# Kernel optimization log

Hardware: AMD Instinct MI355X
Metric: run time of the kernel (lower is better)

## Reference

```python
import jax, jax.numpy as jnp
import numpy as np
from jax import lax

NMS_RADIUS = 4  # module default


def conv2d(x, w, b, pad):
    # x: [B,C,H,W], w: [O,I,kh,kw]
    y = lax.conv_general_dilated(x, w, window_strides=(1, 1),
                                 padding=[(pad, pad), (pad, pad)],
                                 dimension_numbers=('NCHW', 'OIHW', 'NCHW'))
    return y + b[None, :, None, None]


def max_pool(x, r):
    # x: [B,H,W]; kernel (2r+1)x(2r+1), stride 1, pad r (torch pads with -inf)
    k = 2 * r + 1
    return lax.reduce_window(x, -jnp.inf, lax.max,
                             window_dimensions=(1, k, k),
                             window_strides=(1, 1, 1),
                             padding=[(0, 0), (r, r), (r, r)])


def simple_nms(scores, r):
    zeros = jnp.zeros_like(scores)
    max_mask = scores == max_pool(scores, r)
    for _ in range(2):
        supp_mask = max_pool(max_mask.astype(scores.dtype), r) > 0
        supp_scores = jnp.where(supp_mask, zeros, scores)
        new_max_mask = supp_scores == max_pool(supp_scores, r)
        max_mask = max_mask | (new_max_mask & ~supp_mask)
    return jnp.where(max_mask, scores, zeros)


def setup_inputs() -> dict:
    key = jax.random.key(0)
    ks = jax.random.split(key, 7)
    B, Hc, Wc = 16, 60, 80
    x = jax.random.normal(ks[0], (B, 512, Hc, Wc), dtype=jnp.float32)
    wPa = jax.random.normal(ks[1], (256, 512, 3, 3), dtype=jnp.float32) * 0.02
    bPa = jax.random.normal(ks[2], (256,), dtype=jnp.float32) * 0.02
    wPd = jax.random.normal(ks[3], (128, 256, 3, 3), dtype=jnp.float32) * 0.02
    bPd = jax.random.normal(ks[4], (128,), dtype=jnp.float32) * 0.02
    wPg = jax.random.normal(ks[5], (65, 128, 1, 1), dtype=jnp.float32) * 0.02
    bPg = jax.random.normal(ks[6], (65,), dtype=jnp.float32) * 0.02
    return {'x': x, 'wPa': wPa, 'bPa': bPa, 'wPd': wPd, 'bPd': bPd,
            'wPg': wPg, 'bPg': bPg}


def reference(x, wPa, bPa, wPd, bPd, wPg, bPg):
    h1 = jax.nn.relu(conv2d(x, wPa, bPa, pad=1))          # [B,256,Hc,Wc]
    h2 = jax.nn.relu(conv2d(h1, wPd, bPd, pad=1))         # [B,128,Hc,Wc]
    logits = conv2d(h2, wPg, bPg, pad=0)                  # [B,65,Hc,Wc]
    scores = jax.nn.softmax(logits, axis=1)[:, :-1]       # [B,64,Hc,Wc]
    b, _, h, w = scores.shape
    # pixel-unshuffle 8x8 cells -> full resolution
    scores = scores.transpose(0, 2, 3, 1).reshape(b, h, w, 8, 8)
    scores = scores.transpose(0, 1, 3, 2, 4).reshape(b, h * 8, w * 8)
    return simple_nms(scores, NMS_RADIUS)
```

## Files before the change

### kernel.cpp

```cpp
#include <hip/hip_runtime.h>
#include <hip/hip_bf16.h>
#include <math.h>


#define B_      16
#define HC      60
#define WC      80
#define PIX     (HC * WC)
#define HF      480
#define WF      640
#define IMG     (HF * WF)
#define NPIX    (B_ * IMG)

typedef double f64x4 __attribute__((ext_vector_type(4)));

__device__ __forceinline__ int clampi(int v, int lo, int hi) {
    return v < lo ? lo : (v > hi ? hi : v);
}

__global__ __launch_bounds__(256) void cvt_f32_f64(const float* __restrict__ s,
                                                   double* __restrict__ d, int n)
{
    int i = blockIdx.x * 256 + threadIdx.x;
    if (i < n) d[i] = (double)s[i];
}

__global__ __launch_bounds__(256) void prep_w(const float* __restrict__ w,
                                              double* __restrict__ wT,
                                              int CIN, int n)
{
    int i = blockIdx.x * 256 + threadIdx.x;
    if (i >= n) return;
    int cin9 = CIN * 9;
    int oc   = i / cin9;
    int rem  = i - oc * cin9;
    int ic   = rem / 9;
    int dydx = rem - ic * 9;
    size_t dst = ((size_t)((oc >> 4) * (CIN >> 2) + (ic >> 2)) * 9 + dydx) * 64
               + (ic & 3) * 16 + (oc & 15);
    wT[dst] = (double)w[i];
}

template <int CIN, typename TIN, bool RELU>
__global__ __launch_bounds__(256, 4) void conv3x3_mfma(
    const TIN* __restrict__ in,
    const double* __restrict__ wT,
    const double* __restrict__ bias,
    double* __restrict__ out)
{
    const int COUT  = (CIN == 512) ? 256 : 128;
    const int NCH   = CIN / 4;
    const int ytile = blockIdx.x;
    const int ocb   = blockIdx.y;
    const int oc0   = ocb * 16;
    const int b     = blockIdx.z;
    const int tid   = threadIdx.x;
    const int wv    = tid >> 6;
    const int lane  = tid & 63;
    const int q     = lane >> 4;
    const int c     = lane & 15;
    const int y0    = ytile * 4;

    in  += (size_t)b * CIN  * PIX;
    out += (size_t)b * COUT * PIX;

    int rowL[4], colL[4];
    {
        f64x4 pr = (f64x4){0.0, 0.0, 0.0, 0.0};
        double a1 = (lane < 16) ? (double)(16 * lane) : 0.0;
        double b1 = (lane < 16) ? 1.0 : 0.0;
        pr = __builtin_amdgcn_mfma_f64_16x16x4f64(a1, b1, pr, 0, 0, 0);
        double a2 = (lane < 16) ? 1.0 : 0.0;
        double b2 = (lane < 16) ? (double)lane : 0.0;
        pr = __builtin_amdgcn_mfma_f64_16x16x4f64(a2, b2, pr, 0, 0, 0);
#pragma unroll
        for (int i = 0; i < 4; ++i) {
            int code = (int)pr[i];
            rowL[i] = (code >> 4) & 15;
            colL[i] = code & 15;
        }
    }

    __shared__ double smem[2][2544];

    const double* wchunk = wT + (size_t)ocb * NCH * 576;

    f64x4 acc[5];
#pragma unroll
    for (int t = 0; t < 5; ++t) acc[t] = (f64x4){0.0, 0.0, 0.0, 0.0};

    const int bbase = q * 492 + wv * 82 + c;

    int aOff[8];
#pragma unroll
    for (int j = 0; j < 8; ++j) {
        int i   = tid + j * 256;
        int ick = i / 492;
        int rem = i - ick * 492;
        int ry  = rem / 82;
        int rx  = rem - ry * 82;
        int gy  = y0 - 1 + ry, gx = rx - 1;
        bool ok = (i < 1968) && ((unsigned)gy < (unsigned)HC) && ((unsigned)gx < (unsigned)WC);
        aOff[j] = ok ? (ick * PIX + gy * WC + gx) : -1;
    }

    double ra[8];
    double rw0, rw1, rw2;

#define LOADC(ch)                                                              \
    {                                                                          \
        const int gbase = (ch) * 4 * PIX;                                      \
        _Pragma("unroll")                                                      \
        for (int j = 0; j < 8; ++j)                                            \
            ra[j] = (aOff[j] >= 0) ? (double)in[gbase + aOff[j]] : 0.0;        \
        const double* wp = wchunk + (size_t)(ch) * 576;                        \
        rw0 = wp[tid];                                                         \
        rw1 = wp[256 + tid];                                                   \
        rw2 = (tid < 64) ? wp[512 + tid] : 0.0;                                \
    }

#define STOREC(sel)                                                            \
    {                                                                          \
        double* dst = smem[sel];                                               \
        _Pragma("unroll")                                                      \
        for (int j = 0; j < 7; ++j) dst[tid + j * 256] = ra[j];                \
        if (tid < 176) dst[tid + 1792] = ra[7];                                \
        dst[1968 + tid] = rw0;                                                 \
        dst[1968 + 256 + tid] = rw1;                                           \
        if (tid < 64) dst[1968 + 512 + tid] = rw2;                             \
    }

    LOADC(0);
    STOREC(0);
    LOADC(1);
    __syncthreads();

    for (int chk = 0; chk < NCH; ++chk) {
        const int cur = chk & 1;
        if (chk + 1 < NCH) STOREC(cur ^ 1);
        if (chk + 2 < NCH) LOADC(chk + 2);

        const double* act = smem[cur];
        const double* wl  = smem[cur] + 1968;
#pragma unroll
        for (int dy = 0; dy < 3; ++dy) {
#pragma unroll
            for (int dx = 0; dx < 3; ++dx) {
                double a = wl[(dy * 3 + dx) * 64 + lane];
#pragma unroll
                for (int t = 0; t < 5; ++t) {
                    double bv = act[bbase + dy * 82 + t * 16 + dx];
                    acc[t] = __builtin_amdgcn_mfma_f64_16x16x4f64(a, bv, acc[t], 0, 0, 0);
                }
            }
        }
        if (chk + 1 < NCH) __syncthreads();
    }
#undef LOADC
#undef STOREC

    const int y = y0 + wv;
#pragma unroll
    for (int t = 0; t < 5; ++t) {
#pragma unroll
        for (int i = 0; i < 4; ++i) {
            const int oc = oc0 + rowL[i];
            double v = acc[t][i] + bias[oc];
            if (RELU) v = fmax(v, 0.0);
            out[(size_t)oc * PIX + y * WC + t * 16 + colL[i]] = v;
        }
    }
}

__global__ __launch_bounds__(256) void conv1x1_softmax_f64(
    const double* __restrict__ h2,
    const double* __restrict__ wg,
    const double* __restrict__ bg,
    double* __restrict__ S)
{
    int p = blockIdx.x * 256 + threadIdx.x;
    if (p >= PIX) return;
    const int b = blockIdx.y;
    const double* h2p = h2 + (size_t)b * 128 * PIX + p;
    double* Sb = S + (size_t)b * IMG;

    double l[65];
#pragma unroll
    for (int o = 0; o < 65; ++o) l[o] = bg[o];

    for (int icc = 0; icc < 128; icc += 8) {
        double h[8];
#pragma unroll
        for (int k = 0; k < 8; ++k) h[k] = h2p[(size_t)(icc + k) * PIX];
#pragma unroll
        for (int o = 0; o < 65; ++o) {
            const double* wp = wg + o * 128 + icc;
            l[o] += h[0] * wp[0] + h[1] * wp[1] + h[2] * wp[2] + h[3] * wp[3]
                  + h[4] * wp[4] + h[5] * wp[5] + h[6] * wp[6] + h[7] * wp[7];
        }
    }

    double m = l[0];
#pragma unroll
    for (int o = 1; o < 65; ++o) m = fmax(m, l[o]);
    double s = 0.0;
#pragma unroll
    for (int o = 0; o < 65; ++o) { l[o] = exp(l[o] - m); s += l[o]; }
    double inv = 1.0 / s;

    int y = p / WC, x = p % WC;
#pragma unroll
    for (int cy = 0; cy < 8; ++cy)
#pragma unroll
        for (int cx2 = 0; cx2 < 8; ++cx2)
            Sb[(y * 8 + cy) * WF + x * 8 + cx2] = l[cy * 8 + cx2] * inv;
}

__global__ __launch_bounds__(256) void hmax9_f64(const double* __restrict__ in,
                                                 double* __restrict__ out)
{
    int p = blockIdx.x * 256 + threadIdx.x;
    int x = p % WF;
    const double* row = in + (p - x);
    double m = row[x];
#pragma unroll
    for (int d = 1; d <= 4; ++d) {
        m = fmax(m, row[clampi(x - d, 0, WF - 1)]);
        m = fmax(m, row[clampi(x + d, 0, WF - 1)]);
    }
    out[p] = m;
}

__global__ __launch_bounds__(256) void vmax9_eq(const double* __restrict__ T,
                                                const double* __restrict__ S,
                                                unsigned char* __restrict__ M)
{
    int p = blockIdx.x * 256 + threadIdx.x;
    int y = (p % IMG) / WF;
    double m = T[p];
#pragma unroll
    for (int d = 1; d <= 4; ++d) {
        m = fmax(m, T[p + (clampi(y - d, 0, HF - 1) - y) * WF]);
        m = fmax(m, T[p + (clampi(y + d, 0, HF - 1) - y) * WF]);
    }
    M[p] = (S[p] == m) ? (unsigned char)1 : (unsigned char)0;
}

__global__ __launch_bounds__(256) void hor9_u8(const unsigned char* __restrict__ in,
                                               unsigned char* __restrict__ out)
{
    int p = blockIdx.x * 256 + threadIdx.x;
    int x = p % WF;
    const unsigned char* row = in + (p - x);
    unsigned char m = row[x];
#pragma unroll
    for (int d = 1; d <= 4; ++d) {
        m = m | row[clampi(x - d, 0, WF - 1)];
        m = m | row[clampi(x + d, 0, WF - 1)];
    }
    out[p] = m;
}

__global__ __launch_bounds__(256) void vor9_sup(const unsigned char* __restrict__ T8,
                                                unsigned char* __restrict__ SUP)
{
    int p = blockIdx.x * 256 + threadIdx.x;
    int y = (p % IMG) / WF;
    unsigned char m = T8[p];
#pragma unroll
    for (int d = 1; d <= 4; ++d) {
        m = m | T8[p + (clampi(y - d, 0, HF - 1) - y) * WF];
        m = m | T8[p + (clampi(y + d, 0, HF - 1) - y) * WF];
    }
    SUP[p] = m;
}

__global__ __launch_bounds__(256) void hmax9_supp(const double* __restrict__ S,
                                                  const unsigned char* __restrict__ SUP,
                                                  double* __restrict__ T)
{
    int p = blockIdx.x * 256 + threadIdx.x;
    int x = p % WF;
    int base = p - x;
    double m = SUP[p] ? 0.0 : S[p];
#pragma unroll
    for (int d = 1; d <= 4; ++d) {
        int i1 = base + clampi(x - d, 0, WF - 1);
        int i2 = base + clampi(x + d, 0, WF - 1);
        m = fmax(m, SUP[i1] ? 0.0 : S[i1]);
        m = fmax(m, SUP[i2] ? 0.0 : S[i2]);
    }
    T[p] = m;
}

__global__ __launch_bounds__(256) void vmax9_newmask(const double* __restrict__ T,
                                                     const double* __restrict__ S,
                                                     const unsigned char* __restrict__ SUP,
                                                     unsigned char* __restrict__ M)
{
    int p = blockIdx.x * 256 + threadIdx.x;
    int y = (p % IMG) / WF;
    double m = T[p];
#pragma unroll
    for (int d = 1; d <= 4; ++d) {
        m = fmax(m, T[p + (clampi(y - d, 0, HF - 1) - y) * WF]);
        m = fmax(m, T[p + (clampi(y + d, 0, HF - 1) - y) * WF]);
    }
    unsigned char nw = (!SUP[p] && S[p] == m) ? 1 : 0;
    M[p] = M[p] | nw;
}

__global__ __launch_bounds__(256) void final_mask(const double* __restrict__ S,
                                                  const unsigned char* __restrict__ M,
                                                  float* __restrict__ out)
{
    int p = blockIdx.x * 256 + threadIdx.x;
    out[p] = M[p] ? (float)S[p] : 0.f;
}

extern "C" void kernel_launch(void* const* d_in, const int* in_sizes, int n_in,
                              void* d_out, int out_size, void* d_ws, size_t ws_size,
                              hipStream_t stream)
{
    const float* x   = (const float*)d_in[0];
    const float* wPa = (const float*)d_in[1];
    const float* bPa = (const float*)d_in[2];
    const float* wPd = (const float*)d_in[3];
    const float* bPd = (const float*)d_in[4];
    const float* wPg = (const float*)d_in[5];
    const float* bPg = (const float*)d_in[6];
    float* out = (float*)d_out;

    char* ws = (char*)d_ws;
    double*        S   = (double*)(ws);
    double*        T   = (double*)(ws + 39321600);
    unsigned char* M   = (unsigned char*)(ws + 78643200);
    unsigned char* SUP = (unsigned char*)(ws + 83558400);
    unsigned char* T8  = (unsigned char*)(ws + 88473600);
    double* w1t = (double*)(ws + 39321600);
    double* w2t = (double*)(ws + 48758784);
    double* wgd = (double*)(ws + 51118080);
    double* b1d = (double*)(ws + 51184640);
    double* b2d = (double*)(ws + 51186688);
    double* bgd = (double*)(ws + 51187712);
    char*   hbase = ws + 51188736;

    int G = 1;
    for (int g = 16; g >= 1; g >>= 1) {
        if ((size_t)51188736 + (size_t)g * 14745600 <= ws_size) { G = g; break; }
    }

    prep_w<<<(1179648 + 255) / 256, 256, 0, stream>>>(wPa, w1t, 512, 1179648);
    prep_w<<<(294912 + 255) / 256, 256, 0, stream>>>(wPd, w2t, 256, 294912);
    cvt_f32_f64<<<(8320 + 255) / 256, 256, 0, stream>>>(wPg, wgd, 8320);
    cvt_f32_f64<<<1, 256, 0, stream>>>(bPa, b1d, 256);
    cvt_f32_f64<<<1, 256, 0, stream>>>(bPd, b2d, 128);
    cvt_f32_f64<<<1, 256, 0, stream>>>(bPg, bgd, 65);

    for (int bg0 = 0; bg0 < B_; bg0 += G) {
        int Gc = (bg0 + G <= B_) ? G : (B_ - bg0);
        double* h1s = (double*)hbase;
        double* h2s = (double*)(hbase + (size_t)G * 9830400);
        const float* xb = x + (size_t)bg0 * 512 * PIX;
        conv3x3_mfma<512, float, true><<<dim3(15, 16, Gc), 256, 0, stream>>>(xb, w1t, b1d, h1s);
        conv3x3_mfma<256, double, true><<<dim3(15, 8, Gc), 256, 0, stream>>>(h1s, w2t, b2d, h2s);
        conv1x1_softmax_f64<<<dim3(19, Gc), 256, 0, stream>>>(h2s, wgd, bgd, S + (size_t)bg0 * IMG);
    }

    const int NB = NPIX / 256;
    hmax9_f64<<<NB, 256, 0, stream>>>(S, T);
    vmax9_eq<<<NB, 256, 0, stream>>>(T, S, M);
    for (int it = 0; it < 2; ++it) {
        hor9_u8<<<NB, 256, 0, stream>>>(M, T8);
        vor9_sup<<<NB, 256, 0, stream>>>(T8, SUP);
        hmax9_supp<<<NB, 256, 0, stream>>>(S, SUP, T);
        vmax9_newmask<<<NB, 256, 0, stream>>>(T, S, SUP, M);
    }
    final_mask<<<NB, 256, 0, stream>>>(S, M, out);
}
```

Measured before the change: 4.782 ms.

## Retile 3x3 conv blocks to 2 rows by 64 channels with weights read from global

Each conv block now covers 2 output rows and 64 output channels (4 waves: 2 rows × 2 channel-pair groups) instead of 4 rows × 16 channels. Each wave keeps two accumulator sets and reuses every activation fragment across two weight fragments. The aim is to halve shared-memory activation reads per MFMA and cut redundant activation staging across channel blocks. Weights are no longer staged in LDS and are read straight from global memory or cache inside the inner loop. The doubled accumulators raise register pressure, which is why launch bounds drop to 3 blocks per SM.

```diff
diff --git a/kernel.cpp b/kernel.cpp
--- a/kernel.cpp
+++ b/kernel.cpp
@@ -42,7 +42,7 @@
 }
 
 template <int CIN, typename TIN, bool RELU>
-__global__ __launch_bounds__(256, 4) void conv3x3_mfma(
+__global__ __launch_bounds__(256, 3) void conv3x3_mfma(
     const TIN* __restrict__ in,
     const double* __restrict__ wT,
     const double* __restrict__ bias,
@@ -51,15 +51,17 @@
     const int COUT  = (CIN == 512) ? 256 : 128;
     const int NCH   = CIN / 4;
     const int ytile = blockIdx.x;
-    const int ocb   = blockIdx.y;
-    const int oc0   = ocb * 16;
+    const int ocq   = blockIdx.y;
     const int b     = blockIdx.z;
     const int tid   = threadIdx.x;
     const int wv    = tid >> 6;
     const int lane  = tid & 63;
     const int q     = lane >> 4;
     const int c     = lane & 15;
-    const int y0    = ytile * 4;
+    const int wr    = wv & 1;
+    const int wo    = wv >> 1;
+    const int y0    = ytile * 2;
+    const int y     = y0 + wr;
 
     in  += (size_t)b * CIN  * PIX;
     out += (size_t)b * COUT * PIX;
@@ -81,53 +83,49 @@
         }
     }
 
-    __shared__ double smem[2][2544];
-
-    const double* wchunk = wT + (size_t)ocb * NCH * 576;
-
-    f64x4 acc[5];
-#pragma unroll
-    for (int t = 0; t < 5; ++t) acc[t] = (f64x4){0.0, 0.0, 0.0, 0.0};
-
-    const int bbase = q * 492 + wv * 82 + c;
-
-    int aOff[8];
-#pragma unroll
-    for (int j = 0; j < 8; ++j) {
+    __shared__ double smem[2][1312];
+
+    const int ocb0 = ocq * 4 + wo * 2;
+    const double* wA = wT + (size_t)ocb0 * NCH * 576;
+    const double* wB = wT + (size_t)(ocb0 + 1) * NCH * 576;
+
+    f64x4 acc[2][5];
+#pragma unroll
+    for (int o = 0; o < 2; ++o)
+#pragma unroll
+        for (int t = 0; t < 5; ++t) acc[o][t] = (f64x4){0.0, 0.0, 0.0, 0.0};
+
+    const int bbase = q * 328 + wr * 82 + c;
+
+    int aOff[6];
+#pragma unroll
+    for (int j = 0; j < 6; ++j) {
         int i   = tid + j * 256;
-        int ick = i / 492;
-        int rem = i - ick * 492;
+        int ick = i / 328;
+        int rem = i - ick * 328;
         int ry  = rem / 82;
         int rx  = rem - ry * 82;
         int gy  = y0 - 1 + ry, gx = rx - 1;
-        bool ok = (i < 1968) && ((unsigned)gy < (unsigned)HC) && ((unsigned)gx < (unsigned)WC);
+        bool ok = (i < 1312) && ((unsigned)gy < (unsigned)HC) && ((unsigned)gx < (unsigned)WC);
         aOff[j] = ok ? (ick * PIX + gy * WC + gx) : -1;
     }
 
-    double ra[8];
-    double rw0, rw1, rw2;
+    double ra[6];
 
 #define LOADC(ch)                                                              \
     {                                                                          \
         const int gbase = (ch) * 4 * PIX;                                      \
         _Pragma("unroll")                                                      \
-        for (int j = 0; j < 8; ++j)                                            \
+        for (int j = 0; j < 6; ++j)                                            \
             ra[j] = (aOff[j] >= 0) ? (double)in[gbase + aOff[j]] : 0.0;        \
-        const double* wp = wchunk + (size_t)(ch) * 576;                        \
-        rw0 = wp[tid];                                                         \
-        rw1 = wp[256 + tid];                                                   \
-        rw2 = (tid < 64) ? wp[512 + tid] : 0.0;                                \
     }
 
 #define STOREC(sel)                                                            \
     {                                                                          \
         double* dst = smem[sel];                                               \
         _Pragma("unroll")                                                      \
-        for (int j = 0; j < 7; ++j) dst[tid + j * 256] = ra[j];                \
-        if (tid < 176) dst[tid + 1792] = ra[7];                                \
-        dst[1968 + tid] = rw0;                                                 \
-        dst[1968 + 256 + tid] = rw1;                                           \
-        if (tid < 64) dst[1968 + 512 + tid] = rw2;                             \
+        for (int j = 0; j < 5; ++j) dst[tid + j * 256] = ra[j];                \
+        if (tid < 32) dst[1280 + tid] = ra[5];                                 \
     }
 
     LOADC(0);
@@ -140,17 +138,22 @@
         if (chk + 1 < NCH) STOREC(cur ^ 1);
         if (chk + 2 < NCH) LOADC(chk + 2);
 
+        const double* wa  = wA + (size_t)chk * 576;
+        const double* wb  = wB + (size_t)chk * 576;
         const double* act = smem[cur];
-        const double* wl  = smem[cur] + 1968;
+
 #pragma unroll
         for (int dy = 0; dy < 3; ++dy) {
 #pragma unroll
             for (int dx = 0; dx < 3; ++dx) {
-                double a = wl[(dy * 3 + dx) * 64 + lane];
+                const int d = dy * 3 + dx;
+                double a0 = wa[d * 64 + lane];
+                double a1 = wb[d * 64 + lane];
 #pragma unroll
                 for (int t = 0; t < 5; ++t) {
                     double bv = act[bbase + dy * 82 + t * 16 + dx];
-                    acc[t] = __builtin_amdgcn_mfma_f64_16x16x4f64(a, bv, acc[t], 0, 0, 0);
+                    acc[0][t] = __builtin_amdgcn_mfma_f64_16x16x4f64(a0, bv, acc[0][t], 0, 0, 0);
+                    acc[1][t] = __builtin_amdgcn_mfma_f64_16x16x4f64(a1, bv, acc[1][t], 0, 0, 0);
                 }
             }
         }
@@ -159,15 +162,17 @@
 #undef LOADC
 #undef STOREC
 
-    const int y = y0 + wv;
-#pragma unroll
-    for (int t = 0; t < 5; ++t) {
-#pragma unroll
-        for (int i = 0; i < 4; ++i) {
-            const int oc = oc0 + rowL[i];
-            double v = acc[t][i] + bias[oc];
-            if (RELU) v = fmax(v, 0.0);
-            out[(size_t)oc * PIX + y * WC + t * 16 + colL[i]] = v;
+#pragma unroll
+    for (int o = 0; o < 2; ++o) {
+#pragma unroll
+        for (int t = 0; t < 5; ++t) {
+#pragma unroll
+            for (int i = 0; i < 4; ++i) {
+                const int oc = (ocb0 + o) * 16 + rowL[i];
+                double v = acc[o][t][i] + bias[oc];
+                if (RELU) v = fmax(v, 0.0);
+                out[(size_t)oc * PIX + y * WC + t * 16 + colL[i]] = v;
+            }
         }
     }
 }
@@ -362,8 +367,8 @@
         double* h1s = (double*)hbase;
         double* h2s = (double*)(hbase + (size_t)G * 9830400);
         const float* xb = x + (size_t)bg0 * 512 * PIX;
-        conv3x3_mfma<512, float, true><<<dim3(15, 16, Gc), 256, 0, stream>>>(xb, w1t, b1d, h1s);
-        conv3x3_mfma<256, double, true><<<dim3(15, 8, Gc), 256, 0, stream>>>(h1s, w2t, b2d, h2s);
+        conv3x3_mfma<512, float, true><<<dim3(30, 4, Gc), 256, 0, stream>>>(xb, w1t, b1d, h1s);
+        conv3x3_mfma<256, double, true><<<dim3(30, 2, Gc), 256, 0, stream>>>(h1s, w2t, b2d, h2s);
         conv1x1_softmax_f64<<<dim3(19, Gc), 256, 0, stream>>>(h2s, wgd, bgd, S + (size_t)bg0 * IMG);
     }
 
```

Result: faster. 4.471 ms (-6.5%).
